# Kernel tuning notes

Hardware: AMD Instinct MI355X
Metric: run time of the kernel (lower is better)

## Reference

```python
import jax, jax.numpy as jnp
import numpy as np

HEAD_SIZE = 64


def setup_inputs() -> dict:
    key = jax.random.key(0)
    ks = jax.random.split(key, 6)
    B, S, D, H = 8, 2048, 1024, HEAD_SIZE
    return {
        "q": jax.random.normal(ks[0], (B, S, D), dtype=jnp.float32),
        "k": jax.random.normal(ks[1], (B, S, D), dtype=jnp.float32),
        "v": jax.random.normal(ks[2], (B, S, D), dtype=jnp.float32),
        "mask": jnp.ones((B, S), dtype=bool),
        "Wq": jax.random.normal(ks[3], (D, H), dtype=jnp.float32) * (D ** -0.5),
        "Wk": jax.random.normal(ks[4], (D, H), dtype=jnp.float32) * (D ** -0.5),
        "Wv": jax.random.normal(ks[5], (D, H), dtype=jnp.float32) * (D ** -0.5),
    }


def reference(q, k, v, mask, Wq, Wk, Wv):
    # Linear projections (bias=False): x @ W, W is [n_embd, head_size]
    qp = jnp.einsum("bsd,dh->bsh", q, Wq)
    kp = jnp.einsum("bsd,dh->bsh", k, Wk)
    vp = jnp.einsum("bsd,dh->bsh", v, Wv)
    scale = HEAD_SIZE ** -0.5
    scores = jnp.einsum("bqh,bkh->bqk", qp, kp) * scale  # [B, Sq, Sk]
    # 2-D mask [B, Sk] -> broadcast over query dim (mask.unsqueeze(1))
    scores = jnp.where(mask[:, None, :], scores, -jnp.inf)
    attn = jax.nn.softmax(scores, axis=-1)
    # dropout is identity in eval mode (deterministic reference)
    out = jnp.einsum("bqk,bkh->bqh", attn, vp)
    return out
```

## Files before the change

### kernel.cpp

```cpp
#include <hip/hip_runtime.h>
#include <hip/hip_bf16.h>
#include <math.h>

#define B_ 8
#define S_ 2048
#define D_ 1024
#define H_ 64
#define M_ (B_*S_)

typedef __attribute__((ext_vector_type(8))) short bf16x8;
typedef __attribute__((ext_vector_type(8))) unsigned short u16x8;
typedef __attribute__((ext_vector_type(4))) float f32x4;

__device__ inline unsigned short f2bf(float f) {
    unsigned int u = __builtin_bit_cast(unsigned int, f);
    u += 0x7fffu + ((u >> 16) & 1u);
    return (unsigned short)(u >> 16);
}

__global__ __launch_bounds__(256) void mask_kernel(const unsigned char* __restrict__ mask,
                                                   float* __restrict__ mmul, int n) {
    int j = blockIdx.x * 256 + threadIdx.x;
    if (j >= n) return;
    bool boolLayout = mask[1] != 0;
    int mv = boolLayout ? (int)mask[j] : ((const int*)mask)[j];
    mmul[j] = mv ? 1.0f : 0.0f;
}

__global__ __launch_bounds__(256) void wprep_kernel(
    const float* __restrict__ Wq, const float* __restrict__ Wk, const float* __restrict__ Wv,
    unsigned short* __restrict__ Wt)
{
    const int m = blockIdx.y;
    const float* W = (m == 0) ? Wq : (m == 1) ? Wk : Wv;
    unsigned short* Wo = Wt + (size_t)m * 64 * 1024;
    __shared__ unsigned short T[64][65];
    const int t = threadIdx.x;
    const int k0 = blockIdx.x * 64;
    #pragma unroll
    for (int i = 0; i < 16; i++) {
        int vi = t + i * 256;
        int kk = vi >> 6, n = vi & 63;
        T[kk][n] = f2bf(W[(size_t)(k0 + kk) * 64 + n]);
    }
    __syncthreads();
    #pragma unroll
    for (int i = 0; i < 4; i++) {
        int vi = t + i * 256;
        int n = vi >> 4, k4 = vi & 15;
        ushort4 u;
        u.x = T[k4*4+0][n]; u.y = T[k4*4+1][n]; u.z = T[k4*4+2][n]; u.w = T[k4*4+3][n];
        *(ushort4*)&Wo[(size_t)n * 1024 + k0 + k4*4] = u;
    }
}

__global__ __launch_bounds__(256) void proj_kernel(
    const float* __restrict__ q, const float* __restrict__ kx, const float* __restrict__ vx,
    const unsigned short* __restrict__ Wt,
    unsigned short* __restrict__ qp, unsigned short* __restrict__ kp, unsigned short* __restrict__ vp)
{
    const int m = blockIdx.y;
    const float* x = (m == 0) ? q : (m == 1) ? kx : vx;
    const unsigned short* Wm = Wt + (size_t)m * 64 * 1024;
    unsigned short* outp = (m == 0) ? qp : (m == 1) ? kp : vp;

    const int t = threadIdx.x;
    const int w = t >> 6, l = t & 63;
    const int lrow = l & 15, quad = l >> 4;
    const size_t arow = (size_t)(blockIdx.x * 64 + w * 16 + lrow);
    const float* xr = x + arow * D_ + quad * 8;
    const unsigned short* wb = Wm + lrow * 1024 + quad * 8;

    f32x4 acc[4] = {};
    #pragma unroll 4
    for (int k0 = 0; k0 < D_; k0 += 32) {
        float4 a0 = *(const float4*)(xr + k0);
        float4 a1 = *(const float4*)(xr + k0 + 4);
        bf16x8 af;
        af[0] = (short)f2bf(a0.x); af[1] = (short)f2bf(a0.y);
        af[2] = (short)f2bf(a0.z); af[3] = (short)f2bf(a0.w);
        af[4] = (short)f2bf(a1.x); af[5] = (short)f2bf(a1.y);
        af[6] = (short)f2bf(a1.z); af[7] = (short)f2bf(a1.w);
        #pragma unroll
        for (int c = 0; c < 4; c++) {
            bf16x8 bf = *(const bf16x8*)(wb + c * 16 * 1024 + k0);
            acc[c] = __builtin_amdgcn_mfma_f32_16x16x32_bf16(af, bf, acc[c], 0, 0, 0);
        }
    }
    const float sc = (m == 0) ? 0.125f : 1.0f;
    const int orow = blockIdx.x * 64 + w * 16 + quad * 4;
    #pragma unroll
    for (int c = 0; c < 4; c++)
        #pragma unroll
        for (int r = 0; r < 4; r++)
            outp[(size_t)(orow + r) * H_ + c * 16 + lrow] = f2bf(acc[c][r] * sc);
}

__global__ __launch_bounds__(256) void attn_kernel(
    const unsigned short* __restrict__ qp, const unsigned short* __restrict__ kp,
    const unsigned short* __restrict__ vp, const float* __restrict__ mmul,
    float* __restrict__ out)
{
    __shared__ unsigned short Qs[64][72];
    __shared__ unsigned short Ks[64][72];
    __shared__ unsigned short Vt[64][72];
    __shared__ unsigned short Ps[64][72];

    const int t = threadIdx.x;
    const int w = t >> 6, l = t & 63;
    const int lrow = l & 15, lq = l >> 4;
    const int lk8 = lq * 8;
    const int b = blockIdx.y, q0 = blockIdx.x * 64;
    const size_t basebs = (size_t)b * S_;

    const int srow = t >> 3, sc8 = t & 7;

    #pragma unroll
    for (int i = 0; i < 2; i++) {
        u16x8 u = *(const u16x8*)&qp[(basebs + q0 + srow + i*32) * H_ + sc8 * 8];
        *(u16x8*)&Qs[srow + i*32][sc8 * 8] = u;
    }

    u16x8 kr[2], vr[2];
    #pragma unroll
    for (int i = 0; i < 2; i++) {
        kr[i] = *(const u16x8*)&kp[(basebs + srow + i*32) * H_ + sc8 * 8];
        vr[i] = *(const u16x8*)&vp[(basebs + srow + i*32) * H_ + sc8 * 8];
    }

    float lsum[4] = {0.f, 0.f, 0.f, 0.f};
    f32x4 o[4] = {};

    for (int kt = 0; kt < S_ / 64; kt++) {
        __syncthreads();
        #pragma unroll
        for (int i = 0; i < 2; i++) {
            *(u16x8*)&Ks[srow + i*32][sc8 * 8] = kr[i];
            #pragma unroll
            for (int j = 0; j < 8; j++)
                Vt[sc8*8 + j][(srow + i*32) ^ (sc8*8)] = vr[i][j];
        }
        __syncthreads();
        if (kt + 1 < S_/64) {
            const int k0n = (kt + 1) * 64;
            #pragma unroll
            for (int i = 0; i < 2; i++) {
                kr[i] = *(const u16x8*)&kp[(basebs + k0n + srow + i*32) * H_ + sc8 * 8];
                vr[i] = *(const u16x8*)&vp[(basebs + k0n + srow + i*32) * H_ + sc8 * 8];
            }
        }
        const int k0 = kt * 64;
        float mm[4];
        #pragma unroll
        for (int c = 0; c < 4; c++) mm[c] = mmul[basebs + k0 + c*16 + lrow];

        f32x4 s[4] = {};
        #pragma unroll
        for (int kk = 0; kk < 2; kk++) {
            bf16x8 aq = *(const bf16x8*)&Qs[w*16 + lrow][kk*32 + lk8];
            #pragma unroll
            for (int c = 0; c < 4; c++) {
                bf16x8 bk = *(const bf16x8*)&Ks[c*16 + lrow][kk*32 + lk8];
                s[c] = __builtin_amdgcn_mfma_f32_16x16x32_bf16(aq, bk, s[c], 0, 0, 0);
            }
        }
        #pragma unroll
        for (int r = 0; r < 4; r++) {
            float p0 = __expf(s[0][r]) * mm[0];
            float p1 = __expf(s[1][r]) * mm[1];
            float p2 = __expf(s[2][r]) * mm[2];
            float p3 = __expf(s[3][r]) * mm[3];
            lsum[r] += (p0 + p1) + (p2 + p3);
            const int pr = w*16 + lq*4 + r;
            Ps[pr][ 0 + lrow] = f2bf(p0);
            Ps[pr][16 + lrow] = f2bf(p1);
            Ps[pr][32 + lrow] = f2bf(p2);
            Ps[pr][48 + lrow] = f2bf(p3);
        }
        #pragma unroll
        for (int kk = 0; kk < 2; kk++) {
            bf16x8 ap = *(const bf16x8*)&Ps[w*16 + lrow][kk*32 + lk8];
            #pragma unroll
            for (int c = 0; c < 4; c++) {
                const int h = c*16 + lrow;
                const int sw = ((h >> 3) & 7) * 8;
                bf16x8 bv = *(const bf16x8*)&Vt[h][(kk*32 + lk8) ^ sw];
                o[c] = __builtin_amdgcn_mfma_f32_16x16x32_bf16(ap, bv, o[c], 0, 0, 0);
            }
        }
    }

    #pragma unroll
    for (int r = 0; r < 4; r++) {
        #pragma unroll
        for (int d = 1; d < 16; d <<= 1)
            lsum[r] += __shfl_xor(lsum[r], d, 64);
        float inv = 1.0f / lsum[r];
        #pragma unroll
        for (int c = 0; c < 4; c++)
            out[(basebs + q0 + w*16 + lq*4 + r) * H_ + c*16 + lrow] = o[c][r] * inv;
    }
}

extern "C" void kernel_launch(void* const* d_in, const int* in_sizes, int n_in,
                              void* d_out, int out_size, void* d_ws, size_t ws_size,
                              hipStream_t stream) {
    const float* q  = (const float*)d_in[0];
    const float* k  = (const float*)d_in[1];
    const float* v  = (const float*)d_in[2];
    const unsigned char* mask = (const unsigned char*)d_in[3];
    const float* Wq = (const float*)d_in[4];
    const float* Wk = (const float*)d_in[5];
    const float* Wv = (const float*)d_in[6];
    float* out = (float*)d_out;

    unsigned short* qp = (unsigned short*)d_ws;
    unsigned short* kp = qp + (size_t)M_ * H_;
    unsigned short* vp = kp + (size_t)M_ * H_;
    float* mmul = (float*)(vp + (size_t)M_ * H_);
    unsigned short* Wt = (unsigned short*)(mmul + M_);

    wprep_kernel<<<dim3(16, 3), dim3(256), 0, stream>>>(Wq, Wk, Wv, Wt);
    mask_kernel<<<dim3((M_ + 255)/256), dim3(256), 0, stream>>>(mask, mmul, M_);
    proj_kernel<<<dim3(M_/64, 3), dim3(256), 0, stream>>>(q, k, v, Wt, qp, kp, vp);
    attn_kernel<<<dim3(S_/64, B_), dim3(256), 0, stream>>>(qp, kp, vp, mmul, out);
}
```

Before: 265.5 us.

## Split attention over key ranges and software-pipeline projection loads

```diff
diff --git a/kernel.cpp b/kernel.cpp
--- a/kernel.cpp
+++ b/kernel.cpp
@@ -7,6 +7,8 @@
 #define D_ 1024
 #define H_ 64
 #define M_ (B_*S_)
+#define SPLIT 4
+#define KEYS_PER_SPLIT (S_/SPLIT)
 
 typedef __attribute__((ext_vector_type(8))) short bf16x8;
 typedef __attribute__((ext_vector_type(8))) unsigned short u16x8;
@@ -71,21 +73,32 @@
     const float* xr = x + arow * D_ + quad * 8;
     const unsigned short* wb = Wm + lrow * 1024 + quad * 8;
 
+    float4 xa[2], xb[2];
+    bf16x8 wf[2][4];
+    xa[0] = *(const float4*)(xr);
+    xb[0] = *(const float4*)(xr + 4);
+    #pragma unroll
+    for (int c = 0; c < 4; c++) wf[0][c] = *(const bf16x8*)(wb + c * 16 * 1024);
+
     f32x4 acc[4] = {};
-    #pragma unroll 4
-    for (int k0 = 0; k0 < D_; k0 += 32) {
-        float4 a0 = *(const float4*)(xr + k0);
-        float4 a1 = *(const float4*)(xr + k0 + 4);
+    #pragma unroll
+    for (int k0 = 0; k0 < 32; k0++) {
+        const int cur = k0 & 1, nxt = cur ^ 1;
+        if (k0 + 1 < 32) {
+            xa[nxt] = *(const float4*)(xr + (k0 + 1) * 32);
+            xb[nxt] = *(const float4*)(xr + (k0 + 1) * 32 + 4);
+            #pragma unroll
+            for (int c = 0; c < 4; c++)
+                wf[nxt][c] = *(const bf16x8*)(wb + c * 16 * 1024 + (k0 + 1) * 32);
+        }
         bf16x8 af;
-        af[0] = (short)f2bf(a0.x); af[1] = (short)f2bf(a0.y);
-        af[2] = (short)f2bf(a0.z); af[3] = (short)f2bf(a0.w);
-        af[4] = (short)f2bf(a1.x); af[5] = (short)f2bf(a1.y);
-        af[6] = (short)f2bf(a1.z); af[7] = (short)f2bf(a1.w);
-        #pragma unroll
-        for (int c = 0; c < 4; c++) {
-            bf16x8 bf = *(const bf16x8*)(wb + c * 16 * 1024 + k0);
-            acc[c] = __builtin_amdgcn_mfma_f32_16x16x32_bf16(af, bf, acc[c], 0, 0, 0);
-        }
+        af[0] = (short)f2bf(xa[cur].x); af[1] = (short)f2bf(xa[cur].y);
+        af[2] = (short)f2bf(xa[cur].z); af[3] = (short)f2bf(xa[cur].w);
+        af[4] = (short)f2bf(xb[cur].x); af[5] = (short)f2bf(xb[cur].y);
+        af[6] = (short)f2bf(xb[cur].z); af[7] = (short)f2bf(xb[cur].w);
+        #pragma unroll
+        for (int c = 0; c < 4; c++)
+            acc[c] = __builtin_amdgcn_mfma_f32_16x16x32_bf16(af, wf[cur][c], acc[c], 0, 0, 0);
     }
     const float sc = (m == 0) ? 0.125f : 1.0f;
     const int orow = blockIdx.x * 64 + w * 16 + quad * 4;
@@ -99,7 +112,7 @@
 __global__ __launch_bounds__(256) void attn_kernel(
     const unsigned short* __restrict__ qp, const unsigned short* __restrict__ kp,
     const unsigned short* __restrict__ vp, const float* __restrict__ mmul,
-    float* __restrict__ out)
+    float* __restrict__ po, float* __restrict__ pl)
 {
     __shared__ unsigned short Qs[64][72];
     __shared__ unsigned short Ks[64][72];
@@ -111,6 +124,8 @@
     const int lrow = l & 15, lq = l >> 4;
     const int lk8 = lq * 8;
     const int b = blockIdx.y, q0 = blockIdx.x * 64;
+    const int split = blockIdx.z;
+    const int key0 = split * KEYS_PER_SPLIT;
     const size_t basebs = (size_t)b * S_;
 
     const int srow = t >> 3, sc8 = t & 7;
@@ -124,14 +139,14 @@
     u16x8 kr[2], vr[2];
     #pragma unroll
     for (int i = 0; i < 2; i++) {
-        kr[i] = *(const u16x8*)&kp[(basebs + srow + i*32) * H_ + sc8 * 8];
-        vr[i] = *(const u16x8*)&vp[(basebs + srow + i*32) * H_ + sc8 * 8];
+        kr[i] = *(const u16x8*)&kp[(basebs + key0 + srow + i*32) * H_ + sc8 * 8];
+        vr[i] = *(const u16x8*)&vp[(basebs + key0 + srow + i*32) * H_ + sc8 * 8];
     }
 
     float lsum[4] = {0.f, 0.f, 0.f, 0.f};
     f32x4 o[4] = {};
 
-    for (int kt = 0; kt < S_ / 64; kt++) {
+    for (int kt = 0; kt < KEYS_PER_SPLIT / 64; kt++) {
         __syncthreads();
         #pragma unroll
         for (int i = 0; i < 2; i++) {
@@ -141,15 +156,15 @@
                 Vt[sc8*8 + j][(srow + i*32) ^ (sc8*8)] = vr[i][j];
         }
         __syncthreads();
-        if (kt + 1 < S_/64) {
-            const int k0n = (kt + 1) * 64;
+        if (kt + 1 < KEYS_PER_SPLIT / 64) {
+            const int k0n = key0 + (kt + 1) * 64;
             #pragma unroll
             for (int i = 0; i < 2; i++) {
                 kr[i] = *(const u16x8*)&kp[(basebs + k0n + srow + i*32) * H_ + sc8 * 8];
                 vr[i] = *(const u16x8*)&vp[(basebs + k0n + srow + i*32) * H_ + sc8 * 8];
             }
         }
-        const int k0 = kt * 64;
+        const int k0 = key0 + kt * 64;
         float mm[4];
         #pragma unroll
         for (int c = 0; c < 4; c++) mm[c] = mmul[basebs + k0 + c*16 + lrow];
@@ -190,16 +205,39 @@
         }
     }
 
+    float* pob = po + (size_t)split * M_ * H_;
+    float* plb = pl + (size_t)split * M_;
     #pragma unroll
     for (int r = 0; r < 4; r++) {
         #pragma unroll
         for (int d = 1; d < 16; d <<= 1)
             lsum[r] += __shfl_xor(lsum[r], d, 64);
-        float inv = 1.0f / lsum[r];
+        const size_t row = basebs + q0 + w*16 + lq*4 + r;
+        if (lrow == 0) plb[row] = lsum[r];
         #pragma unroll
         for (int c = 0; c < 4; c++)
-            out[(basebs + q0 + w*16 + lq*4 + r) * H_ + c*16 + lrow] = o[c][r] * inv;
-    }
+            pob[row * H_ + c*16 + lrow] = o[c][r];
+    }
+}
+
+__global__ __launch_bounds__(256) void combine_kernel(
+    const float* __restrict__ po, const float* __restrict__ pl, float* __restrict__ out)
+{
+    const int idx = blockIdx.x * 256 + threadIdx.x;
+    const size_t row = idx >> 4;
+    const int c4 = (idx & 15) * 4;
+    float lt = 0.f;
+    #pragma unroll
+    for (int s = 0; s < SPLIT; s++) lt += pl[(size_t)s * M_ + row];
+    f32x4 acc = {};
+    #pragma unroll
+    for (int s = 0; s < SPLIT; s++) {
+        const f32x4 p = *(const f32x4*)&po[((size_t)s * M_ + row) * H_ + c4];
+        acc += p;
+    }
+    const float inv = 1.0f / lt;
+    f32x4 r = acc * inv;
+    *(f32x4*)&out[row * H_ + c4] = r;
 }
 
 extern "C" void kernel_launch(void* const* d_in, const int* in_sizes, int n_in,
@@ -219,9 +257,12 @@
     unsigned short* vp = kp + (size_t)M_ * H_;
     float* mmul = (float*)(vp + (size_t)M_ * H_);
     unsigned short* Wt = (unsigned short*)(mmul + M_);
+    float* po = (float*)(Wt + (size_t)3 * 64 * 1024);
+    float* pl = po + (size_t)SPLIT * M_ * H_;
 
     wprep_kernel<<<dim3(16, 3), dim3(256), 0, stream>>>(Wq, Wk, Wv, Wt);
     mask_kernel<<<dim3((M_ + 255)/256), dim3(256), 0, stream>>>(mask, mmul, M_);
     proj_kernel<<<dim3(M_/64, 3), dim3(256), 0, stream>>>(q, k, v, Wt, qp, kp, vp);
-    attn_kernel<<<dim3(S_/64, B_), dim3(256), 0, stream>>>(qp, kp, vp, mmul, out);
-}
+    attn_kernel<<<dim3(S_/64, B_, SPLIT), dim3(256), 0, stream>>>(qp, kp, vp, mmul, po, pl);
+    combine_kernel<<<dim3(M_*16/256), dim3(256), 0, stream>>>(po, pl, out);
+}
```

Result: faster. 259.9 us (-2.1%).
